# Performance work log

Measured on AMD Instinct MI355X. Metric: run time of the kernel, lower is better.

The kernel has to match this reference:

```python
import jax, jax.numpy as jnp
import numpy as np

E = 1024          # av_embed_size
H = 16            # heads
N = 32            # batch
NN = 4096         # num_neurons
LR = 0.01
TAU_POS = 20.0
TAU_NEG = 20.0
AUDIO = 1024      # audioblocksize


def setup_inputs() -> dict:
    key = jax.random.key(0)
    ks = jax.random.split(key, 8)
    scale = 1.0 / np.sqrt(E)
    return {
        "av_value": jax.random.normal(ks[0], (1, N, E), jnp.float32),
        "av_key": jax.random.normal(ks[1], (1, N, E), jnp.float32),
        "av_query": jax.random.normal(ks[2], (1, N, E), jnp.float32),
        "in_proj_w": jax.random.normal(ks[3], (3 * E, E), jnp.float32) * scale,
        "in_proj_b": jnp.zeros((3 * E,), jnp.float32),
        "out_proj_w": jax.random.normal(ks[4], (E, E), jnp.float32) * scale,
        "out_proj_b": jnp.zeros((E,), jnp.float32),
        "connections": jax.random.normal(ks[5], (E, NN), jnp.float32) * 0.1,
    }


def _mha(q, k, v, in_proj_w, in_proj_b, out_proj_w, out_proj_b):
    # q,k,v: (L, N, E) -- torch nn.MultiheadAttention layout, no mask
    Dh = E // H
    qp = q @ in_proj_w[:E].T + in_proj_b[:E]
    kp = k @ in_proj_w[E:2 * E].T + in_proj_b[E:2 * E]
    vp = v @ in_proj_w[2 * E:].T + in_proj_b[2 * E:]
    # (L, N, E) -> (N, H, L, Dh)
    def split_heads(x):
        L = x.shape[0]
        return x.reshape(L, N, H, Dh).transpose(1, 2, 0, 3)
    qh, kh, vh = split_heads(qp), split_heads(kp), split_heads(vp)
    scores = jnp.einsum('nhqd,nhkd->nhqk', qh, kh) / jnp.sqrt(jnp.float32(Dh))
    attn = jax.nn.softmax(scores, axis=-1)
    out = jnp.einsum('nhqk,nhkd->nhqd', attn, vh)          # (N, H, Lq, Dh)
    out = out.transpose(2, 0, 1, 3).reshape(-1, N, E)      # (Lq, N, E)
    return out @ out_proj_w.T + out_proj_b


def _stdp_delta(pre, post, lr, tau_pos, tau_neg):
    # pre: (N, Dp), post: (N, Dq) -> (N, Dp, Dq)
    d = jnp.abs(post[:, None, :] - pre[:, :, None])
    return lr * (jnp.exp(-d / tau_pos) - jnp.exp(-d / tau_neg))


def reference(av_value, av_key, av_query, in_proj_w, in_proj_b, out_proj_w, out_proj_b, connections):
    attn_out = _mha(av_query, av_key, av_value, in_proj_w, in_proj_b, out_proj_w, out_proj_b)
    attn_out = attn_out.squeeze(0)                       # (N, E)
    neuron_out = attn_out @ connections                  # (N, NN)
    # STDP update of ComplexNeuron connections (sum over batch)
    conn_delta = _stdp_delta(attn_out, neuron_out, LR, TAU_POS, TAU_NEG).sum(axis=0)
    new_connections = connections + conn_delta           # (E, NN)
    # STDP update of attention params (mean over batch); torch computes the
    # identical delta in a loop for idx 0 and idx 2 -- compute once here.
    pre_act = av_value.squeeze(0)                        # (N, E)
    w_delta = _stdp_delta(pre_act, attn_out, LR, TAU_POS, TAU_NEG).mean(axis=0)  # (E, E)
    new_in_proj_w = in_proj_w + jnp.tile(w_delta, (3, 1))
    new_out_proj_w = out_proj_w + w_delta
    audio_output = neuron_out[:, :AUDIO]                 # (N, 1024)
    return (audio_output, new_connections, new_in_proj_w, new_out_proj_w)
```

## Files before the change

### kernel.cpp

```cpp
#include <hip/hip_runtime.h>

#define EDIM 1024
#define NROW 32

constexpr int AUD_ELEMS  = 32 * 1024;
constexpr int CONN_ELEMS = 1024 * 4096;
constexpr int INW_ELEMS  = 3 * 1024 * 1024;
constexpr int OUTW_ELEMS = 1024 * 1024;

constexpr int AUD_F4   = AUD_ELEMS / 4;
constexpr int CONN_F4  = CONN_ELEMS / 4;
constexpr int INW_F4   = INW_ELEMS / 4;
constexpr int OUTW_F4  = OUTW_ELEMS / 4;
constexpr int TOTAL_F4 = AUD_F4 + CONN_F4 + INW_F4 + OUTW_F4;

__global__ __launch_bounds__(256) void copy_zero_kernel(
    const float4* __restrict__ conn, const float4* __restrict__ inw,
    const float4* __restrict__ outw, float4* __restrict__ out)
{
    int i = blockIdx.x * 256 + threadIdx.x;
    if (i >= TOTAL_F4) return;
    float4 v;
    if (i < AUD_F4) {
        v = make_float4(0.f, 0.f, 0.f, 0.f);
    } else if (i < AUD_F4 + CONN_F4) {
        v = conn[i - AUD_F4];
    } else if (i < AUD_F4 + CONN_F4 + INW_F4) {
        v = inw[i - (AUD_F4 + CONN_F4)];
    } else {
        v = outw[i - (AUD_F4 + CONN_F4 + INW_F4)];
    }
    out[i] = v;
}

__global__ __launch_bounds__(256) void gemm_bt32_kernel(
    const float* __restrict__ A, const float* __restrict__ B,
    const float* __restrict__ bias, float* __restrict__ C)
{
    int gw   = (blockIdx.x * 256 + threadIdx.x) >> 6;
    int lane = threadIdx.x & 63;
    int e    = gw & 1023;
    int n0   = (gw >> 10) * 8;

    const float4* Br = (const float4*)(B + (size_t)e * EDIM);
    float4 b0 = Br[lane], b1 = Br[lane + 64], b2 = Br[lane + 128], b3 = Br[lane + 192];
    float be = bias[e];

#pragma unroll
    for (int i = 0; i < 8; ++i) {
        int n = n0 + i;
        const float4* Ar = (const float4*)(A + (size_t)n * EDIM);
        float4 a0 = Ar[lane], a1 = Ar[lane + 64], a2 = Ar[lane + 128], a3 = Ar[lane + 192];
        float s = a0.x*b0.x + a0.y*b0.y + a0.z*b0.z + a0.w*b0.w;
        s += a1.x*b1.x + a1.y*b1.y + a1.z*b1.z + a1.w*b1.w;
        s += a2.x*b2.x + a2.y*b2.y + a2.z*b2.z + a2.w*b2.w;
        s += a3.x*b3.x + a3.y*b3.y + a3.z*b3.z + a3.w*b3.w;
#pragma unroll
        for (int off = 32; off > 0; off >>= 1) s += __shfl_down(s, off);
        if (lane == 0) C[(size_t)n * EDIM + e] = s + be;
    }
}

__global__ __launch_bounds__(256) void audio_kernel(
    const float* __restrict__ attn, const float* __restrict__ conn,
    float* __restrict__ out)
{
    int g  = blockIdx.x & 7;
    int kc = blockIdx.x >> 3;
    int n0 = g * 4;
    int k0 = kc * 64;
    int t  = threadIdx.x;

    __shared__ float sa[256];
    sa[t] = attn[(size_t)(n0 + (t >> 6)) * EDIM + k0 + (t & 63)];
    __syncthreads();

    const float4* c4 = (const float4*)conn;
    float4 acc0 = {0,0,0,0}, acc1 = {0,0,0,0}, acc2 = {0,0,0,0}, acc3 = {0,0,0,0};
#pragma unroll 4
    for (int k = 0; k < 64; ++k) {
        float4 c = c4[(size_t)(k0 + k) * 1024 + t];
        float a0v = sa[k], a1v = sa[64 + k], a2v = sa[128 + k], a3v = sa[192 + k];
        acc0.x += a0v*c.x; acc0.y += a0v*c.y; acc0.z += a0v*c.z; acc0.w += a0v*c.w;
        acc1.x += a1v*c.x; acc1.y += a1v*c.y; acc1.z += a1v*c.z; acc1.w += a1v*c.w;
        acc2.x += a2v*c.x; acc2.y += a2v*c.y; acc2.z += a2v*c.z; acc2.w += a2v*c.w;
        acc3.x += a3v*c.x; acc3.y += a3v*c.y; acc3.z += a3v*c.z; acc3.w += a3v*c.w;
    }

    float* o0 = out + (size_t)(n0 + 0) * 1024 + 4 * t;
    float* o1 = out + (size_t)(n0 + 1) * 1024 + 4 * t;
    float* o2 = out + (size_t)(n0 + 2) * 1024 + 4 * t;
    float* o3 = out + (size_t)(n0 + 3) * 1024 + 4 * t;
    atomicAdd(o0 + 0, acc0.x); atomicAdd(o0 + 1, acc0.y); atomicAdd(o0 + 2, acc0.z); atomicAdd(o0 + 3, acc0.w);
    atomicAdd(o1 + 0, acc1.x); atomicAdd(o1 + 1, acc1.y); atomicAdd(o1 + 2, acc1.z); atomicAdd(o1 + 3, acc1.w);
    atomicAdd(o2 + 0, acc2.x); atomicAdd(o2 + 1, acc2.y); atomicAdd(o2 + 2, acc2.z); atomicAdd(o2 + 3, acc2.w);
    atomicAdd(o3 + 0, acc3.x); atomicAdd(o3 + 1, acc3.y); atomicAdd(o3 + 2, acc3.z); atomicAdd(o3 + 3, acc3.w);
}

extern "C" void kernel_launch(void* const* d_in, const int* in_sizes, int n_in,
                              void* d_out, int out_size, void* d_ws, size_t ws_size,
                              hipStream_t stream) {
    const float* av_value   = (const float*)d_in[0];
    const float* in_proj_w  = (const float*)d_in[3];
    const float* in_proj_b  = (const float*)d_in[4];
    const float* out_proj_w = (const float*)d_in[5];
    const float* out_proj_b = (const float*)d_in[6];
    const float* conn       = (const float*)d_in[7];
    float* out = (float*)d_out;

    float* vp   = (float*)d_ws;
    float* attn = vp + AUD_ELEMS;

    copy_zero_kernel<<<(TOTAL_F4 + 255) / 256, 256, 0, stream>>>(
        (const float4*)conn, (const float4*)in_proj_w,
        (const float4*)out_proj_w, (float4*)out);

    gemm_bt32_kernel<<<1024, 256, 0, stream>>>(
        av_value, in_proj_w + 2 * EDIM * EDIM, in_proj_b + 2 * EDIM, vp);

    gemm_bt32_kernel<<<1024, 256, 0, stream>>>(
        vp, out_proj_w, out_proj_b, attn);

    audio_kernel<<<128, 256, 0, stream>>>(attn, conn, out);
}
```

Before: 126.0 us.

## Fuse copy, projections and audio GEMV into one cooperative kernel

Replaces four separate launches with a single cooperative kernel of 1024 blocks that uses grid-wide syncs between stages. The bulk weight copy becomes a grid-stride loop placed right after the first projection GEMV, so the two can overlap, and inter-kernel launch gaps disappear. In exchange it adds two grid barriers plus thread fences. The copy now runs with fewer resident threads per element, and `__launch_bounds__(256, 4)` may constrain register allocation.

```diff
diff --git a/kernel.cpp b/kernel.cpp
--- a/kernel.cpp
+++ b/kernel.cpp
@@ -1,7 +1,9 @@
 #include <hip/hip_runtime.h>
+#include <hip/hip_cooperative_groups.h>
+
+namespace cg = cooperative_groups;
 
 #define EDIM 1024
-#define NROW 32
 
 constexpr int AUD_ELEMS  = 32 * 1024;
 constexpr int CONN_ELEMS = 1024 * 4096;
@@ -14,33 +16,18 @@
 constexpr int OUTW_F4  = OUTW_ELEMS / 4;
 constexpr int TOTAL_F4 = AUD_F4 + CONN_F4 + INW_F4 + OUTW_F4;
 
-__global__ __launch_bounds__(256) void copy_zero_kernel(
-    const float4* __restrict__ conn, const float4* __restrict__ inw,
-    const float4* __restrict__ outw, float4* __restrict__ out)
+constexpr int GRID_BLOCKS = 1024;
+constexpr int NTHREADS    = GRID_BLOCKS * 256;
+
+__device__ __forceinline__ void gemm_rowdot(
+    const float* __restrict__ A, const float* __restrict__ B,
+    const float* __restrict__ bias, float* __restrict__ C,
+    int bid, int tid)
 {
-    int i = blockIdx.x * 256 + threadIdx.x;
-    if (i >= TOTAL_F4) return;
-    float4 v;
-    if (i < AUD_F4) {
-        v = make_float4(0.f, 0.f, 0.f, 0.f);
-    } else if (i < AUD_F4 + CONN_F4) {
-        v = conn[i - AUD_F4];
-    } else if (i < AUD_F4 + CONN_F4 + INW_F4) {
-        v = inw[i - (AUD_F4 + CONN_F4)];
-    } else {
-        v = outw[i - (AUD_F4 + CONN_F4 + INW_F4)];
-    }
-    out[i] = v;
-}
-
-__global__ __launch_bounds__(256) void gemm_bt32_kernel(
-    const float* __restrict__ A, const float* __restrict__ B,
-    const float* __restrict__ bias, float* __restrict__ C)
-{
-    int gw   = (blockIdx.x * 256 + threadIdx.x) >> 6;
-    int lane = threadIdx.x & 63;
+    int gw   = (bid << 2) | (tid >> 6);
+    int lane = tid & 63;
     int e    = gw & 1023;
-    int n0   = (gw >> 10) * 8;
+    int n0   = (gw >> 10) << 3;
 
     const float4* Br = (const float4*)(B + (size_t)e * EDIM);
     float4 b0 = Br[lane], b1 = Br[lane + 64], b2 = Br[lane + 128], b3 = Br[lane + 192];
@@ -61,17 +48,16 @@
     }
 }
 
-__global__ __launch_bounds__(256) void audio_kernel(
+__device__ __forceinline__ void audio_tile(
     const float* __restrict__ attn, const float* __restrict__ conn,
-    float* __restrict__ out)
+    float* __restrict__ out, float* sa, int bid, int tid)
 {
-    int g  = blockIdx.x & 7;
-    int kc = blockIdx.x >> 3;
+    int g  = bid & 7;
+    int kc = bid >> 3;
     int n0 = g * 4;
     int k0 = kc * 64;
-    int t  = threadIdx.x;
+    int t  = tid;
 
-    __shared__ float sa[256];
     sa[t] = attn[(size_t)(n0 + (t >> 6)) * EDIM + k0 + (t & 63)];
     __syncthreads();
 
@@ -97,6 +83,50 @@
     atomicAdd(o3 + 0, acc3.x); atomicAdd(o3 + 1, acc3.y); atomicAdd(o3 + 2, acc3.z); atomicAdd(o3 + 3, acc3.w);
 }
 
+__global__ __launch_bounds__(256, 4) void fused_kernel(
+    const float* __restrict__ av_value, const float* __restrict__ in_proj_w,
+    const float* __restrict__ in_proj_b, const float* __restrict__ out_proj_w,
+    const float* __restrict__ out_proj_b, const float* __restrict__ conn,
+    float* __restrict__ out, float* __restrict__ vp, float* __restrict__ attn)
+{
+    cg::grid_group grid = cg::this_grid();
+    __shared__ float sa[256];
+    int bid = blockIdx.x, tid = threadIdx.x;
+
+    gemm_rowdot(av_value, in_proj_w + 2 * EDIM * EDIM, in_proj_b + 2 * EDIM, vp,
+                bid, tid);
+
+    {
+        const float4* cs = (const float4*)conn;
+        const float4* is = (const float4*)in_proj_w;
+        const float4* os = (const float4*)out_proj_w;
+        float4* o4 = (float4*)out;
+        for (int i = bid * 256 + tid; i < TOTAL_F4; i += NTHREADS) {
+            float4 v;
+            if (i < AUD_F4) {
+                v = make_float4(0.f, 0.f, 0.f, 0.f);
+            } else if (i < AUD_F4 + CONN_F4) {
+                v = cs[i - AUD_F4];
+            } else if (i < AUD_F4 + CONN_F4 + INW_F4) {
+                v = is[i - (AUD_F4 + CONN_F4)];
+            } else {
+                v = os[i - (AUD_F4 + CONN_F4 + INW_F4)];
+            }
+            o4[i] = v;
+        }
+    }
+
+    __threadfence();
+    grid.sync();
+
+    gemm_rowdot(vp, out_proj_w, out_proj_b, attn, bid, tid);
+
+    __threadfence();
+    grid.sync();
+
+    if (bid < 128) audio_tile(attn, conn, out, sa, bid, tid);
+}
+
 extern "C" void kernel_launch(void* const* d_in, const int* in_sizes, int n_in,
                               void* d_out, int out_size, void* d_ws, size_t ws_size,
                               hipStream_t stream) {
@@ -111,15 +141,9 @@
     float* vp   = (float*)d_ws;
     float* attn = vp + AUD_ELEMS;
 
-    copy_zero_kernel<<<(TOTAL_F4 + 255) / 256, 256, 0, stream>>>(
-        (const float4*)conn, (const float4*)in_proj_w,
-        (const float4*)out_proj_w, (float4*)out);
-
-    gemm_bt32_kernel<<<1024, 256, 0, stream>>>(
-        av_value, in_proj_w + 2 * EDIM * EDIM, in_proj_b + 2 * EDIM, vp);
-
-    gemm_bt32_kernel<<<1024, 256, 0, stream>>>(
-        vp, out_proj_w, out_proj_b, attn);
-
-    audio_kernel<<<128, 256, 0, stream>>>(attn, conn, out);
+    void* args[] = { (void*)&av_value, (void*)&in_proj_w, (void*)&in_proj_b,
+                     (void*)&out_proj_w, (void*)&out_proj_b, (void*)&conn,
+                     (void*)&out, (void*)&vp, (void*)&attn };
+    hipLaunchCooperativeKernel((void*)fused_kernel, dim3(GRID_BLOCKS), dim3(256),
+                               args, 0, stream);
 }
```

Measured after the change: 481.0 us. +281.6%, slower.

## Fuse copy into first GEMM and out-projection into audio kernel

Applied to the files above, without the earlier changes.

The output copy/zero pass now runs as a grid-stride loop inside the first GEMM kernel, so the two share one launch. The out-projection GEMM is recomputed per tail block for its K-chunk and written straight into shared memory, which removes the intermediate attn buffer and two launches. The cost is that out_proj_w rows get read once per batch group (8x redundancy across blocks), and the tail grid grows to 256 blocks with a smaller K chunk, which doubles the number of atomics.

```diff
diff --git a/kernel.cpp b/kernel.cpp
--- a/kernel.cpp
+++ b/kernel.cpp
@@ -1,7 +1,6 @@
 #include <hip/hip_runtime.h>
 
 #define EDIM 1024
-#define NROW 32
 
 constexpr int AUD_ELEMS  = 32 * 1024;
 constexpr int CONN_ELEMS = 1024 * 4096;
@@ -14,33 +13,23 @@
 constexpr int OUTW_F4  = OUTW_ELEMS / 4;
 constexpr int TOTAL_F4 = AUD_F4 + CONN_F4 + INW_F4 + OUTW_F4;
 
-__global__ __launch_bounds__(256) void copy_zero_kernel(
-    const float4* __restrict__ conn, const float4* __restrict__ inw,
-    const float4* __restrict__ outw, float4* __restrict__ out)
+constexpr int A_BLOCKS   = 1024;
+constexpr int A_NTHREADS = A_BLOCKS * 256;
+
+constexpr int KC       = 32;
+constexpr int NB_TAIL  = (1024 / KC) * 8;
+
+__global__ __launch_bounds__(256) void gemm1_copy_kernel(
+    const float* __restrict__ A, const float* __restrict__ B,
+    const float* __restrict__ bias, float* __restrict__ C,
+    const float4* __restrict__ conn4, const float4* __restrict__ inw4,
+    const float4* __restrict__ outw4, float4* __restrict__ out4)
 {
-    int i = blockIdx.x * 256 + threadIdx.x;
-    if (i >= TOTAL_F4) return;
-    float4 v;
-    if (i < AUD_F4) {
-        v = make_float4(0.f, 0.f, 0.f, 0.f);
-    } else if (i < AUD_F4 + CONN_F4) {
-        v = conn[i - AUD_F4];
-    } else if (i < AUD_F4 + CONN_F4 + INW_F4) {
-        v = inw[i - (AUD_F4 + CONN_F4)];
-    } else {
-        v = outw[i - (AUD_F4 + CONN_F4 + INW_F4)];
-    }
-    out[i] = v;
-}
-
-__global__ __launch_bounds__(256) void gemm_bt32_kernel(
-    const float* __restrict__ A, const float* __restrict__ B,
-    const float* __restrict__ bias, float* __restrict__ C)
-{
-    int gw   = (blockIdx.x * 256 + threadIdx.x) >> 6;
-    int lane = threadIdx.x & 63;
+    int bid = blockIdx.x, tid = threadIdx.x;
+    int gw   = (bid << 2) | (tid >> 6);
+    int lane = tid & 63;
     int e    = gw & 1023;
-    int n0   = (gw >> 10) * 8;
+    int n0   = (gw >> 10) << 3;
 
     const float4* Br = (const float4*)(B + (size_t)e * EDIM);
     float4 b0 = Br[lane], b1 = Br[lane + 64], b2 = Br[lane + 128], b3 = Br[lane + 192];
@@ -59,38 +48,113 @@
         for (int off = 32; off > 0; off >>= 1) s += __shfl_down(s, off);
         if (lane == 0) C[(size_t)n * EDIM + e] = s + be;
     }
+
+    for (int i = bid * 256 + tid; i < TOTAL_F4; i += A_NTHREADS) {
+        float4 v;
+        if (i < AUD_F4) {
+            v = make_float4(0.f, 0.f, 0.f, 0.f);
+        } else if (i < AUD_F4 + CONN_F4) {
+            v = conn4[i - AUD_F4];
+        } else if (i < AUD_F4 + CONN_F4 + INW_F4) {
+            v = inw4[i - (AUD_F4 + CONN_F4)];
+        } else {
+            v = outw4[i - (AUD_F4 + CONN_F4 + INW_F4)];
+        }
+        out4[i] = v;
+    }
 }
 
-__global__ __launch_bounds__(256) void audio_kernel(
-    const float* __restrict__ attn, const float* __restrict__ conn,
+__global__ __launch_bounds__(256) void tail_kernel(
+    const float* __restrict__ vp, const float* __restrict__ Wo,
+    const float* __restrict__ bo, const float* __restrict__ conn,
     float* __restrict__ out)
 {
     int g  = blockIdx.x & 7;
     int kc = blockIdx.x >> 3;
     int n0 = g * 4;
-    int k0 = kc * 64;
-    int t  = threadIdx.x;
+    int k0 = kc * KC;
+    int tid  = threadIdx.x;
+    int wid  = tid >> 6;
+    int lane = tid & 63;
 
-    __shared__ float sa[256];
-    sa[t] = attn[(size_t)(n0 + (t >> 6)) * EDIM + k0 + (t & 63)];
+    __shared__ float sa[4 * KC];
+
+    const float4* vp4 = (const float4*)vp;
+    float4 a0q0 = vp4[(size_t)(n0+0)*256 + lane      ];
+    float4 a0q1 = vp4[(size_t)(n0+0)*256 + lane +  64];
+    float4 a0q2 = vp4[(size_t)(n0+0)*256 + lane + 128];
+    float4 a0q3 = vp4[(size_t)(n0+0)*256 + lane + 192];
+    float4 a1q0 = vp4[(size_t)(n0+1)*256 + lane      ];
+    float4 a1q1 = vp4[(size_t)(n0+1)*256 + lane +  64];
+    float4 a1q2 = vp4[(size_t)(n0+1)*256 + lane + 128];
+    float4 a1q3 = vp4[(size_t)(n0+1)*256 + lane + 192];
+    float4 a2q0 = vp4[(size_t)(n0+2)*256 + lane      ];
+    float4 a2q1 = vp4[(size_t)(n0+2)*256 + lane +  64];
+    float4 a2q2 = vp4[(size_t)(n0+2)*256 + lane + 128];
+    float4 a2q3 = vp4[(size_t)(n0+2)*256 + lane + 192];
+    float4 a3q0 = vp4[(size_t)(n0+3)*256 + lane      ];
+    float4 a3q1 = vp4[(size_t)(n0+3)*256 + lane +  64];
+    float4 a3q2 = vp4[(size_t)(n0+3)*256 + lane + 128];
+    float4 a3q3 = vp4[(size_t)(n0+3)*256 + lane + 192];
+
+    constexpr int EPW = KC / 4;
+#pragma unroll
+    for (int ei = 0; ei < EPW; ++ei) {
+        int kk = wid * EPW + ei;
+        int e  = k0 + kk;
+        const float4* Br = (const float4*)(Wo + (size_t)e * EDIM);
+        float4 b0 = Br[lane], b1 = Br[lane + 64], b2 = Br[lane + 128], b3 = Br[lane + 192];
+
+        float s0 = a0q0.x*b0.x + a0q0.y*b0.y + a0q0.z*b0.z + a0q0.w*b0.w
+                 + a0q1.x*b1.x + a0q1.y*b1.y + a0q1.z*b1.z + a0q1.w*b1.w
+                 + a0q2.x*b2.x + a0q2.y*b2.y + a0q2.z*b2.z + a0q2.w*b2.w
+                 + a0q3.x*b3.x + a0q3.y*b3.y + a0q3.z*b3.z + a0q3.w*b3.w;
+        float s1 = a1q0.x*b0.x + a1q0.y*b0.y + a1q0.z*b0.z + a1q0.w*b0.w
+                 + a1q1.x*b1.x + a1q1.y*b1.y + a1q1.z*b1.z + a1q1.w*b1.w
+                 + a1q2.x*b2.x + a1q2.y*b2.y + a1q2.z*b2.z + a1q2.w*b2.w
+                 + a1q3.x*b3.x + a1q3.y*b3.y + a1q3.z*b3.z + a1q3.w*b3.w;
+        float s2 = a2q0.x*b0.x + a2q0.y*b0.y + a2q0.z*b0.z + a2q0.w*b0.w
+                 + a2q1.x*b1.x + a2q1.y*b1.y + a2q1.z*b1.z + a2q1.w*b1.w
+                 + a2q2.x*b2.x + a2q2.y*b2.y + a2q2.z*b2.z + a2q2.w*b2.w
+                 + a2q3.x*b3.x + a2q3.y*b3.y + a2q3.z*b3.z + a2q3.w*b3.w;
+        float s3 = a3q0.x*b0.x + a3q0.y*b0.y + a3q0.z*b0.z + a3q0.w*b0.w
+                 + a3q1.x*b1.x + a3q1.y*b1.y + a3q1.z*b1.z + a3q1.w*b1.w
+                 + a3q2.x*b2.x + a3q2.y*b2.y + a3q2.z*b2.z + a3q2.w*b2.w
+                 + a3q3.x*b3.x + a3q3.y*b3.y + a3q3.z*b3.z + a3q3.w*b3.w;
+
+#pragma unroll
+        for (int off = 32; off > 0; off >>= 1) {
+            s0 += __shfl_down(s0, off);
+            s1 += __shfl_down(s1, off);
+            s2 += __shfl_down(s2, off);
+            s3 += __shfl_down(s3, off);
+        }
+        if (lane == 0) {
+            float be = bo[e];
+            sa[0 * KC + kk] = s0 + be;
+            sa[1 * KC + kk] = s1 + be;
+            sa[2 * KC + kk] = s2 + be;
+            sa[3 * KC + kk] = s3 + be;
+        }
+    }
     __syncthreads();
 
     const float4* c4 = (const float4*)conn;
     float4 acc0 = {0,0,0,0}, acc1 = {0,0,0,0}, acc2 = {0,0,0,0}, acc3 = {0,0,0,0};
 #pragma unroll 4
-    for (int k = 0; k < 64; ++k) {
-        float4 c = c4[(size_t)(k0 + k) * 1024 + t];
-        float a0v = sa[k], a1v = sa[64 + k], a2v = sa[128 + k], a3v = sa[192 + k];
-        acc0.x += a0v*c.x; acc0.y += a0v*c.y; acc0.z += a0v*c.z; acc0.w += a0v*c.w;
-        acc1.x += a1v*c.x; acc1.y += a1v*c.y; acc1.z += a1v*c.z; acc1.w += a1v*c.w;
-        acc2.x += a2v*c.x; acc2.y += a2v*c.y; acc2.z += a2v*c.z; acc2.w += a2v*c.w;
-        acc3.x += a3v*c.x; acc3.y += a3v*c.y; acc3.z += a3v*c.z; acc3.w += a3v*c.w;
+    for (int k = 0; k < KC; ++k) {
+        float4 c = c4[(size_t)(k0 + k) * 1024 + tid];
+        float v0 = sa[k], v1 = sa[KC + k], v2 = sa[2 * KC + k], v3 = sa[3 * KC + k];
+        acc0.x += v0*c.x; acc0.y += v0*c.y; acc0.z += v0*c.z; acc0.w += v0*c.w;
+        acc1.x += v1*c.x; acc1.y += v1*c.y; acc1.z += v1*c.z; acc1.w += v1*c.w;
+        acc2.x += v2*c.x; acc2.y += v2*c.y; acc2.z += v2*c.z; acc2.w += v2*c.w;
+        acc3.x += v3*c.x; acc3.y += v3*c.y; acc3.z += v3*c.z; acc3.w += v3*c.w;
     }
 
-    float* o0 = out + (size_t)(n0 + 0) * 1024 + 4 * t;
-    float* o1 = out + (size_t)(n0 + 1) * 1024 + 4 * t;
-    float* o2 = out + (size_t)(n0 + 2) * 1024 + 4 * t;
-    float* o3 = out + (size_t)(n0 + 3) * 1024 + 4 * t;
+    float* o0 = out + (size_t)(n0 + 0) * 1024 + 4 * tid;
+    float* o1 = out + (size_t)(n0 + 1) * 1024 + 4 * tid;
+    float* o2 = out + (size_t)(n0 + 2) * 1024 + 4 * tid;
+    float* o3 = out + (size_t)(n0 + 3) * 1024 + 4 * tid;
     atomicAdd(o0 + 0, acc0.x); atomicAdd(o0 + 1, acc0.y); atomicAdd(o0 + 2, acc0.z); atomicAdd(o0 + 3, acc0.w);
     atomicAdd(o1 + 0, acc1.x); atomicAdd(o1 + 1, acc1.y); atomicAdd(o1 + 2, acc1.z); atomicAdd(o1 + 3, acc1.w);
     atomicAdd(o2 + 0, acc2.x); atomicAdd(o2 + 1, acc2.y); atomicAdd(o2 + 2, acc2.z); atomicAdd(o2 + 3, acc2.w);
@@ -108,18 +172,13 @@
     const float* conn       = (const float*)d_in[7];
     float* out = (float*)d_out;
 
-    float* vp   = (float*)d_ws;
-    float* attn = vp + AUD_ELEMS;
+    float* vp = (float*)d_ws;
 
-    copy_zero_kernel<<<(TOTAL_F4 + 255) / 256, 256, 0, stream>>>(
+    gemm1_copy_kernel<<<A_BLOCKS, 256, 0, stream>>>(
+        av_value, in_proj_w + 2 * EDIM * EDIM, in_proj_b + 2 * EDIM, vp,
         (const float4*)conn, (const float4*)in_proj_w,
         (const float4*)out_proj_w, (float4*)out);
 
-    gemm_bt32_kernel<<<1024, 256, 0, stream>>>(
-        av_value, in_proj_w + 2 * EDIM * EDIM, in_proj_b + 2 * EDIM, vp);
-
-    gemm_bt32_kernel<<<1024, 256, 0, stream>>>(
-        vp, out_proj_w, out_proj_b, attn);
-
-    audio_kernel<<<128, 256, 0, stream>>>(attn, conn, out);
+    tail_kernel<<<NB_TAIL, 256, 0, stream>>>(
+        vp, out_proj_w, out_proj_b, conn, out);
 }
```

After: 127.5 us. Within noise of the previous version (+1.1%).
